# Kernel optimization log

Hardware: AMD Instinct MI355X
Metric: run time of the kernel (lower is better)

The kernel has to match this reference:

```python
import jax, jax.numpy as jnp
import numpy as np

B, T, C = 2, 4096, 512
H = 8
MEMORY = 256  # window: key j visible to query i iff 0 <= i - j <= MEMORY


def setup_inputs() -> dict:
    key = jax.random.key(0)
    k1, k2, k3 = jax.random.split(key, 3)
    x = jax.random.normal(k1, (B, T, C), dtype=jnp.float32)
    w_attn = jax.random.normal(k2, (3 * C, C), dtype=jnp.float32) * 0.02
    w_proj = jax.random.normal(k3, (C, C), dtype=jnp.float32) * 0.02
    return {"x": x, "w_attn": w_attn, "w_proj": w_proj}


def reference(x, w_attn, w_proj):
    b, t, c = x.shape
    d = c // H
    # fused QKV projection (Linear without bias): x @ W^T
    qkv = jnp.einsum('btc,fc->btf', x, w_attn)  # [B,T,3C]
    q, k, v = jnp.split(qkv, 3, axis=-1)
    # [B,T,C] -> [B,H,T,d]
    q = q.reshape(b, t, H, d).transpose(0, 2, 1, 3)
    k = k.reshape(b, t, H, d).transpose(0, 2, 1, 3)
    v = v.reshape(b, t, H, d).transpose(0, 2, 1, 3)
    # sliding-window causal mask: tril(0) & ~tril(-memory-1)
    i = jnp.arange(t)[:, None]
    j = jnp.arange(t)[None, :]
    mask = (j <= i) & (i - j <= MEMORY)  # [T,T] bool
    scores = jnp.einsum('bhqd,bhkd->bhqk', q, k) * (1.0 / np.sqrt(d))
    scores = jnp.where(mask, scores, -jnp.inf)
    attn = jax.nn.softmax(scores, axis=-1)
    y = jnp.einsum('bhqk,bhkd->bhqd', attn, v)  # [B,H,T,d]
    y = y.transpose(0, 2, 1, 3).reshape(b, t, c)
    # output projection
    y = jnp.einsum('btc,fc->btf', y, w_proj)
    return y
```

## Files before the change

kernel.cpp:

```cpp
#include <hip/hip_runtime.h>
#include <hip/hip_bf16.h>
#include <stdint.h>

#define BB 2
#define TT 4096
#define CC 512
#define HH 8
#define MEM 256

typedef unsigned short u16;
typedef __bf16 bf16x8 __attribute__((ext_vector_type(8)));
typedef float floatx4 __attribute__((ext_vector_type(4)));

__device__ inline u16 f2bf(float f) {
  uint32_t u = __float_as_uint(f);
  uint32_t r = (u + 0x7fffu + ((u >> 16) & 1u)) >> 16;
  return (u16)r;
}
__device__ inline u16 f2bf_r(float f) {
  return (u16)((__float_as_uint(f) + 0x8000u) >> 16);
}

__device__ inline void gld16(const u16* g, u16* lds) {
  __builtin_amdgcn_global_load_lds(
      (const __attribute__((address_space(1))) uint32_t*)g,
      (__attribute__((address_space(3))) uint32_t*)lds, 16, 0, 0);
}

__global__ __launch_bounds__(256) void cvt_all(const float* __restrict__ x,
                                               const float* __restrict__ wa,
                                               const float* __restrict__ wp,
                                               u16* __restrict__ xb,
                                               u16* __restrict__ wab,
                                               u16* __restrict__ wpb) {
  int i = blockIdx.x * 256 + threadIdx.x;
  const float* s; u16* d; int off;
  if (i < 1048576) { s = x; d = xb; off = i; }
  else if (i < 1245184) { s = wa; d = wab; off = i - 1048576; }
  else { s = wp; d = wpb; off = i - 1245184; }
  float4 v = *reinterpret_cast<const float4*>(s + (size_t)off * 4);
  ushort4 o;
  o.x = f2bf(v.x); o.y = f2bf(v.y); o.z = f2bf(v.z); o.w = f2bf(v.w);
  *reinterpret_cast<ushort4*>(d + (size_t)off * 4) = o;
}

template <bool OUT_F32>
__global__ __launch_bounds__(256) void gemm_bt(const u16* __restrict__ A,
                                               const u16* __restrict__ Bw,
                                               void* __restrict__ Cout,
                                               int M, int N, int K) {
  __shared__ __align__(16) u16 As[128 * 32];
  __shared__ __align__(16) u16 Bs[128 * 32];
  const int tid = threadIdx.x;
  const int w = tid >> 6, lane = tid & 63, quad = lane >> 4, l16 = lane & 15;
  const int wm = w >> 1, wn = w & 1;
  const int m0 = blockIdx.x * 128, n0 = blockIdx.y * 128;

  floatx4 acc[4][4] = {};
  const int nK = K >> 5;
  for (int kb = 0; kb < nK; ++kb) {
    const int kof = kb * 32;
    {
      int c = tid;
      gld16(A + (size_t)(m0 + (c >> 2)) * K + kof + (c & 3) * 8, As + (size_t)c * 8);
      c = tid + 256;
      gld16(A + (size_t)(m0 + (c >> 2)) * K + kof + (c & 3) * 8, As + (size_t)c * 8);
      c = tid;
      gld16(Bw + (size_t)(n0 + (c >> 2)) * K + kof + (c & 3) * 8, Bs + (size_t)c * 8);
      c = tid + 256;
      gld16(Bw + (size_t)(n0 + (c >> 2)) * K + kof + (c & 3) * 8, Bs + (size_t)c * 8);
    }
    __syncthreads();
    bf16x8 af[4], bfr[4];
#pragma unroll
    for (int i = 0; i < 4; i++)
      af[i] = *reinterpret_cast<const bf16x8*>(&As[(wm * 64 + i * 16 + l16) * 32 + quad * 8]);
#pragma unroll
    for (int i = 0; i < 4; i++)
      bfr[i] = *reinterpret_cast<const bf16x8*>(&Bs[(wn * 64 + i * 16 + l16) * 32 + quad * 8]);
#pragma unroll
    for (int mi = 0; mi < 4; mi++)
#pragma unroll
      for (int ni = 0; ni < 4; ni++)
        acc[mi][ni] = __builtin_amdgcn_mfma_f32_16x16x32_bf16(af[mi], bfr[ni], acc[mi][ni], 0, 0, 0);
    __syncthreads();
  }
#pragma unroll
  for (int mi = 0; mi < 4; mi++) {
    int row = m0 + wm * 64 + mi * 16 + quad * 4;
#pragma unroll
    for (int ni = 0; ni < 4; ni++) {
      int col = n0 + wn * 64 + ni * 16 + l16;
#pragma unroll
      for (int r = 0; r < 4; r++) {
        if (OUT_F32)
          ((float*)Cout)[(size_t)(row + r) * N + col] = acc[mi][ni][r];
        else
          ((u16*)Cout)[(size_t)(row + r) * N + col] = f2bf(acc[mi][ni][r]);
      }
    }
  }
}

__global__ __launch_bounds__(256) void gemm_bt_n64(const u16* __restrict__ A,
                                                   const u16* __restrict__ Bw,
                                                   float* __restrict__ C,
                                                   int M, int N, int K) {
  __shared__ __align__(16) u16 As[128 * 32];
  __shared__ __align__(16) u16 Bs[64 * 32];
  const int tid = threadIdx.x;
  const int w = tid >> 6, lane = tid & 63, quad = lane >> 4, l16 = lane & 15;
  const int m0 = blockIdx.x * 128, n0 = blockIdx.y * 64;

  floatx4 acc[2][4] = {};
  const int nK = K >> 5;
  for (int kb = 0; kb < nK; ++kb) {
    const int kof = kb * 32;
    {
      int c = tid;
      gld16(A + (size_t)(m0 + (c >> 2)) * K + kof + (c & 3) * 8, As + (size_t)c * 8);
      c = tid + 256;
      gld16(A + (size_t)(m0 + (c >> 2)) * K + kof + (c & 3) * 8, As + (size_t)c * 8);
      c = tid;
      gld16(Bw + (size_t)(n0 + (c >> 2)) * K + kof + (c & 3) * 8, Bs + (size_t)c * 8);
    }
    __syncthreads();
    bf16x8 af[2], bfr[4];
#pragma unroll
    for (int i = 0; i < 2; i++)
      af[i] = *reinterpret_cast<const bf16x8*>(&As[(w * 32 + i * 16 + l16) * 32 + quad * 8]);
#pragma unroll
    for (int i = 0; i < 4; i++)
      bfr[i] = *reinterpret_cast<const bf16x8*>(&Bs[(i * 16 + l16) * 32 + quad * 8]);
#pragma unroll
    for (int mi = 0; mi < 2; mi++)
#pragma unroll
      for (int ni = 0; ni < 4; ni++)
        acc[mi][ni] = __builtin_amdgcn_mfma_f32_16x16x32_bf16(af[mi], bfr[ni], acc[mi][ni], 0, 0, 0);
    __syncthreads();
  }
#pragma unroll
  for (int mi = 0; mi < 2; mi++) {
    int row = m0 + w * 32 + mi * 16 + quad * 4;
#pragma unroll
    for (int ni = 0; ni < 4; ni++) {
      int col = n0 + ni * 16 + l16;
#pragma unroll
      for (int r = 0; r < 4; r++)
        C[(size_t)(row + r) * N + col] = acc[mi][ni][r];
    }
  }
}

__global__ __launch_bounds__(256, 2) void attn_win(const u16* __restrict__ qkv,
                                                   u16* __restrict__ y) {
  const int q0 = blockIdx.x * 128;
  const int h = blockIdx.y;
  const int b = blockIdx.z;
  const int tid = threadIdx.x;
  const int w = tid >> 6, lane = tid & 63, quad = lane >> 4, l16 = lane & 15;

  __shared__ __align__(16) u16 Qs[128 * 64];
  __shared__ __align__(16) u16 Ks[64 * 64];
  __shared__ __align__(16) u16 Vt[64 * 72];
  __shared__ __align__(16) u16 Ps[4][32 * 72];

  const size_t baseQ = ((size_t)(b * TT + q0)) * 1536 + h * 64;
#pragma unroll
  for (int j = 0; j < 4; j++) {
    int c = tid + j * 256, row = c >> 3, blk = (c & 7) ^ (row & 7);
    gld16(qkv + baseQ + (size_t)row * 1536 + blk * 8, Qs + (size_t)c * 8);
  }
  __syncthreads();
  bf16x8 qf[2][2];
#pragma unroll
  for (int mi = 0; mi < 2; mi++) {
    int row = w * 32 + mi * 16 + l16;
    qf[mi][0] = *reinterpret_cast<const bf16x8*>(&Qs[row * 64 + (quad ^ (l16 & 7)) * 8]);
    qf[mi][1] = *reinterpret_cast<const bf16x8*>(&Qs[row * 64 + ((quad + 4) ^ (l16 & 7)) * 8]);
#pragma unroll
    for (int e = 0; e < 8; e++) {
      qf[mi][0][e] = qf[mi][0][e] * (__bf16)0.125f;
      qf[mi][1][e] = qf[mi][1][e] * (__bf16)0.125f;
    }
  }

  floatx4 acc_o[2][4] = {};
  float l_acc[2][4] = {{0.f, 0.f, 0.f, 0.f}, {0.f, 0.f, 0.f, 0.f}};

  const int s_min = (q0 >= 256) ? 0 : ((256 - q0) >> 6);
  const int key_v = tid >> 3, dc_v = tid & 7;
  const int key_v1 = (tid + 256) >> 3, dc_v1 = tid & 7;

  uint4 vp0, vp1;
  {
    size_t baseV = ((size_t)(b * TT + (q0 - 256 + s_min * 64))) * 1536 + 1024 + h * 64;
    vp0 = *reinterpret_cast<const uint4*>(qkv + baseV + (size_t)key_v * 1536 + dc_v * 8);
    vp1 = *reinterpret_cast<const uint4*>(qkv + baseV + (size_t)key_v1 * 1536 + dc_v1 * 8);
  }

  for (int s = s_min; s < 6; ++s) {
    const int k0 = q0 - 256 + s * 64;
    const size_t baseK = ((size_t)(b * TT + k0)) * 1536 + 512 + h * 64;
    {
      int c = tid, row = c >> 3, blk = (c & 7) ^ (row & 7);
      gld16(qkv + baseK + (size_t)row * 1536 + blk * 8, Ks + (size_t)c * 8);
      c = tid + 256; row = c >> 3; blk = (c & 7) ^ (row & 7);
      gld16(qkv + baseK + (size_t)row * 1536 + blk * 8, Ks + (size_t)c * 8);
    }
    {
      u16 tmp[8];
      *reinterpret_cast<uint4*>(tmp) = vp0;
      int col = key_v ^ (dc_v * 8);
#pragma unroll
      for (int e = 0; e < 8; e++) Vt[(dc_v * 8 + e) * 72 + col] = tmp[e];
      *reinterpret_cast<uint4*>(tmp) = vp1;
      col = key_v1 ^ (dc_v1 * 8);
#pragma unroll
      for (int e = 0; e < 8; e++) Vt[(dc_v1 * 8 + e) * 72 + col] = tmp[e];
    }
    if (s < 5) {
      size_t baseV = ((size_t)(b * TT + k0 + 64)) * 1536 + 1024 + h * 64;
      vp0 = *reinterpret_cast<const uint4*>(qkv + baseV + (size_t)key_v * 1536 + dc_v * 8);
      vp1 = *reinterpret_cast<const uint4*>(qkv + baseV + (size_t)key_v1 * 1536 + dc_v1 * 8);
    }
    __syncthreads();

    int mode = 0;
    if (s == 0) mode = (w < 2) ? 1 : 3;
    else if (s == 1) mode = (w < 2) ? 0 : 1;
    else if (s == 4) mode = (w < 2) ? 2 : 0;
    else if (s == 5) mode = (w < 2) ? 3 : 2;

    if (mode != 3) {
      bf16x8 bfr[4][2];
#pragma unroll
      for (int nt = 0; nt < 4; nt++) {
        int krow = nt * 16 + l16;
        bfr[nt][0] = *reinterpret_cast<const bf16x8*>(&Ks[krow * 64 + (quad ^ (l16 & 7)) * 8]);
        bfr[nt][1] = *reinterpret_cast<const bf16x8*>(&Ks[krow * 64 + ((quad + 4) ^ (l16 & 7)) * 8]);
      }
      floatx4 sc[2][4] = {};
#pragma unroll
      for (int mi = 0; mi < 2; mi++)
#pragma unroll
        for (int nt = 0; nt < 4; nt++) {
          sc[mi][nt] = __builtin_amdgcn_mfma_f32_16x16x32_bf16(qf[mi][0], bfr[nt][0], sc[mi][nt], 0, 0, 0);
          sc[mi][nt] = __builtin_amdgcn_mfma_f32_16x16x32_bf16(qf[mi][1], bfr[nt][1], sc[mi][nt], 0, 0, 0);
        }
      const int hqb = (w & 1) * 32 + quad * 4;
      if (mode == 1) {
#pragma unroll
        for (int mi = 0; mi < 2; mi++)
#pragma unroll
          for (int nt = 0; nt < 4; nt++)
#pragma unroll
            for (int r = 0; r < 4; r++)
              if (hqb + mi * 16 + r > nt * 16 + l16) sc[mi][nt][r] = -1e30f;
      } else if (mode == 2) {
#pragma unroll
        for (int mi = 0; mi < 2; mi++)
#pragma unroll
          for (int nt = 0; nt < 4; nt++)
#pragma unroll
            for (int r = 0; r < 4; r++)
              if (hqb + mi * 16 + r < nt * 16 + l16) sc[mi][nt][r] = -1e30f;
      }
#pragma unroll
      for (int mi = 0; mi < 2; mi++)
#pragma unroll
        for (int nt = 0; nt < 4; nt++)
#pragma unroll
          for (int r = 0; r < 4; r++) {
            float p = __expf(sc[mi][nt][r] - 4.0f);
            l_acc[mi][r] += p;
            Ps[w][(mi * 16 + quad * 4 + r) * 72 + nt * 16 + l16] = f2bf_r(p);
          }
#pragma unroll
      for (int mi = 0; mi < 2; mi++)
#pragma unroll
        for (int ki = 0; ki < 2; ki++) {
          bf16x8 pf = *reinterpret_cast<const bf16x8*>(
              &Ps[w][(mi * 16 + l16) * 72 + ki * 32 + quad * 8]);
#pragma unroll
          for (int nt = 0; nt < 4; nt++) {
            int d = nt * 16 + l16;
            bf16x8 vf = *reinterpret_cast<const bf16x8*>(
                &Vt[d * 72 + ((ki * 32 + quad * 8) ^ (d & 56))]);
            acc_o[mi][nt] = __builtin_amdgcn_mfma_f32_16x16x32_bf16(pf, vf, acc_o[mi][nt], 0, 0, 0);
          }
        }
    }
    __syncthreads();
  }
#pragma unroll
  for (int mi = 0; mi < 2; mi++)
#pragma unroll
    for (int r = 0; r < 4; r++) {
      float l = l_acc[mi][r];
      l += __shfl_xor(l, 1);
      l += __shfl_xor(l, 2);
      l += __shfl_xor(l, 4);
      l += __shfl_xor(l, 8);
      float inv = 1.f / l;
      int row = q0 + w * 32 + mi * 16 + quad * 4 + r;
      size_t base = (size_t)(b * TT + row) * 512 + h * 64;
#pragma unroll
      for (int nt = 0; nt < 4; nt++)
        y[base + nt * 16 + l16] = f2bf(acc_o[mi][nt][r] * inv);
    }
}

extern "C" void kernel_launch(void* const* d_in, const int* in_sizes, int n_in,
                              void* d_out, int out_size, void* d_ws, size_t ws_size,
                              hipStream_t stream) {
  const float* x = (const float*)d_in[0];
  const float* w_attn = (const float*)d_in[1];
  const float* w_proj = (const float*)d_in[2];
  float* out = (float*)d_out;

  u16* xb = (u16*)d_ws;
  u16* wab = xb + (size_t)8192 * 512;
  u16* wpb = wab + (size_t)1536 * 512;
  u16* qkv = wpb + (size_t)512 * 512;
  u16* yb = qkv + (size_t)8192 * 1536;

  cvt_all<<<5120, 256, 0, stream>>>(x, w_attn, w_proj, xb, wab, wpb);
  gemm_bt<false><<<dim3(64, 12), 256, 0, stream>>>(xb, wab, (void*)qkv, 8192, 1536, 512);
  attn_win<<<dim3(TT / 128, HH, BB), 256, 0, stream>>>(qkv, yb);
  gemm_bt_n64<<<dim3(64, 8), 256, 0, stream>>>(yb, wpb, out, 8192, 512, 512);
}
```

Measured before the change: 126.0 us.

## Replace QKV GEMM with 256x256 double-buffered, swizzled, phase-pipelined MFMA kernel

The 128x128 single-buffered QKV GEMM is replaced by a 512-thread kernel computing 256x256 tiles with BK=64. It double-buffers LDS, staging half-tiles across four compute phases so global loads overlap MFMA work. It also XOR-swizzles LDS to avoid bank conflicts, raises wave priority around the MFMA block, and remaps block IDs across XCDs. The tradeoffs are only 192 workgroups on a large-CU GPU, heavy LDS (128KB per block), and many more accumulator registers.

```diff
diff --git a/kernel.cpp b/kernel.cpp
--- a/kernel.cpp
+++ b/kernel.cpp
@@ -26,6 +26,8 @@
       (const __attribute__((address_space(1))) uint32_t*)g,
       (__attribute__((address_space(3))) uint32_t*)lds, 16, 0, 0);
 }
+
+#define BARM() asm volatile("" ::: "memory")
 
 __global__ __launch_bounds__(256) void cvt_all(const float* __restrict__ x,
                                                const float* __restrict__ wa,
@@ -44,60 +46,124 @@
   *reinterpret_cast<ushort4*>(d + (size_t)off * 4) = o;
 }
 
-template <bool OUT_F32>
-__global__ __launch_bounds__(256) void gemm_bt(const u16* __restrict__ A,
-                                               const u16* __restrict__ Bw,
-                                               void* __restrict__ Cout,
-                                               int M, int N, int K) {
-  __shared__ __align__(16) u16 As[128 * 32];
-  __shared__ __align__(16) u16 Bs[128 * 32];
+__device__ inline void stage_hA(const u16* __restrict__ G, u16* lds, int K,
+                                int gr0, int koff, int half, int wv, int lane) {
+#pragma unroll
+  for (int j = 0; j < 2; j++) {
+    int lrow = (j * 8 + wv) * 8 + (lane >> 3);
+    int row = (lrow & 63) + ((lrow >> 6) << 7) + (half << 6);
+    int blk = (lane & 7) ^ (row & 7);
+    gld16(G + (size_t)(gr0 + row) * K + koff + blk * 8,
+          lds + (size_t)row * 64 + (lane & 7) * 8);
+  }
+}
+__device__ inline void stage_hB(const u16* __restrict__ G, u16* lds, int K,
+                                int gr0, int koff, int half, int wv, int lane) {
+#pragma unroll
+  for (int j = 0; j < 2; j++) {
+    int lrow = (j * 8 + wv) * 8 + (lane >> 3);
+    int row = (lrow & 31) + ((lrow >> 5) << 6) + (half << 5);
+    int blk = (lane & 7) ^ (row & 7);
+    gld16(G + (size_t)(gr0 + row) * K + koff + blk * 8,
+          lds + (size_t)row * 64 + (lane & 7) * 8);
+  }
+}
+
+#define PHASE(MQ, NQ, STAGE, WAITV)                                            \
+  {                                                                            \
+    bf16x8 af[4][2], bfv[2][2];                                                \
+    _Pragma("unroll") for (int fm = 0; fm < 4; fm++) {                         \
+      int row = wm * 128 + MQ * 64 + fm * 16 + l16;                            \
+      const u16* p = Ad + (size_t)row * 64;                                    \
+      af[fm][0] = *(const bf16x8*)(p + ((quad ^ (row & 7)) << 3));             \
+      af[fm][1] = *(const bf16x8*)(p + (((4 + quad) ^ (row & 7)) << 3));       \
+    }                                                                          \
+    _Pragma("unroll") for (int fn = 0; fn < 2; fn++) {                         \
+      int row = wn * 64 + NQ * 32 + fn * 16 + l16;                             \
+      const u16* p = Bd + (size_t)row * 64;                                    \
+      bfv[fn][0] = *(const bf16x8*)(p + ((quad ^ (row & 7)) << 3));            \
+      bfv[fn][1] = *(const bf16x8*)(p + (((4 + quad) ^ (row & 7)) << 3));      \
+    }                                                                          \
+    STAGE;                                                                     \
+    BARM();                                                                    \
+    __builtin_amdgcn_s_barrier();                                              \
+    asm volatile("s_waitcnt lgkmcnt(0)" ::: "memory");                         \
+    __builtin_amdgcn_sched_barrier(0);                                         \
+    __builtin_amdgcn_s_setprio(1);                                             \
+    _Pragma("unroll") for (int fm = 0; fm < 4; fm++)                           \
+      _Pragma("unroll") for (int fn = 0; fn < 2; fn++) {                       \
+        acc[MQ * 4 + fm][NQ * 2 + fn] =                                        \
+            __builtin_amdgcn_mfma_f32_16x16x32_bf16(                           \
+                af[fm][0], bfv[fn][0], acc[MQ * 4 + fm][NQ * 2 + fn], 0, 0, 0);\
+        acc[MQ * 4 + fm][NQ * 2 + fn] =                                        \
+            __builtin_amdgcn_mfma_f32_16x16x32_bf16(                           \
+                af[fm][1], bfv[fn][1], acc[MQ * 4 + fm][NQ * 2 + fn], 0, 0, 0);\
+      }                                                                        \
+    __builtin_amdgcn_s_setprio(0);                                             \
+    WAITV;                                                                     \
+    BARM();                                                                    \
+    __builtin_amdgcn_s_barrier();                                              \
+    BARM();                                                                    \
+  }
+
+__global__ __launch_bounds__(512, 2) void gemm256(const u16* __restrict__ A,
+                                                  const u16* __restrict__ Bw,
+                                                  u16* __restrict__ C,
+                                                  int M, int N, int K) {
+  __shared__ __align__(16) u16 As[2][256 * 64];
+  __shared__ __align__(16) u16 Bs[2][256 * 64];
   const int tid = threadIdx.x;
-  const int w = tid >> 6, lane = tid & 63, quad = lane >> 4, l16 = lane & 15;
-  const int wm = w >> 1, wn = w & 1;
-  const int m0 = blockIdx.x * 128, n0 = blockIdx.y * 128;
-
-  floatx4 acc[4][4] = {};
-  const int nK = K >> 5;
-  for (int kb = 0; kb < nK; ++kb) {
-    const int kof = kb * 32;
-    {
-      int c = tid;
-      gld16(A + (size_t)(m0 + (c >> 2)) * K + kof + (c & 3) * 8, As + (size_t)c * 8);
-      c = tid + 256;
-      gld16(A + (size_t)(m0 + (c >> 2)) * K + kof + (c & 3) * 8, As + (size_t)c * 8);
-      c = tid;
-      gld16(Bw + (size_t)(n0 + (c >> 2)) * K + kof + (c & 3) * 8, Bs + (size_t)c * 8);
-      c = tid + 256;
-      gld16(Bw + (size_t)(n0 + (c >> 2)) * K + kof + (c & 3) * 8, Bs + (size_t)c * 8);
-    }
-    __syncthreads();
-    bf16x8 af[4], bfr[4];
-#pragma unroll
-    for (int i = 0; i < 4; i++)
-      af[i] = *reinterpret_cast<const bf16x8*>(&As[(wm * 64 + i * 16 + l16) * 32 + quad * 8]);
-#pragma unroll
-    for (int i = 0; i < 4; i++)
-      bfr[i] = *reinterpret_cast<const bf16x8*>(&Bs[(wn * 64 + i * 16 + l16) * 32 + quad * 8]);
-#pragma unroll
-    for (int mi = 0; mi < 4; mi++)
-#pragma unroll
-      for (int ni = 0; ni < 4; ni++)
-        acc[mi][ni] = __builtin_amdgcn_mfma_f32_16x16x32_bf16(af[mi], bfr[ni], acc[mi][ni], 0, 0, 0);
-    __syncthreads();
-  }
-#pragma unroll
-  for (int mi = 0; mi < 4; mi++) {
-    int row = m0 + wm * 64 + mi * 16 + quad * 4;
+  const int lane = tid & 63, wv = tid >> 6;
+  const int quad = lane >> 4, l16 = lane & 15;
+  const int wm = wv >> 2, wn = wv & 3;
+
+  const int nbx = N >> 8;
+  const int nwg = (M >> 8) * nbx;
+  int wg = blockIdx.x;
+  if ((nwg & 7) == 0) wg = (wg & 7) * (nwg >> 3) + (wg >> 3);
+  const int m0 = (wg / nbx) << 8, n0 = (wg % nbx) << 8;
+
+  const int nK = K >> 6;
+  floatx4 acc[8][4] = {};
+
+  stage_hA(A, As[0], K, m0, 0, 0, wv, lane);
+  stage_hA(A, As[0], K, m0, 0, 1, wv, lane);
+  stage_hB(Bw, Bs[0], K, n0, 0, 0, wv, lane);
+  stage_hB(Bw, Bs[0], K, n0, 0, 1, wv, lane);
+  if (nK > 1) {
+    stage_hA(A, As[1], K, m0, 64, 0, wv, lane);
+    stage_hB(Bw, Bs[1], K, n0, 64, 0, wv, lane);
+    asm volatile("s_waitcnt vmcnt(4)" ::: "memory");
+  } else {
+    asm volatile("s_waitcnt vmcnt(0)" ::: "memory");
+  }
+  BARM();
+  __builtin_amdgcn_s_barrier();
+  BARM();
+
+  for (int t = 0; t < nK; ++t) {
+    const int d = t & 1;
+    u16* Ad = As[d]; u16* Bd = Bs[d];
+    u16* An = As[d ^ 1]; u16* Bn = Bs[d ^ 1];
+    const int k1 = (t + 1) << 6, k2 = (t + 2) << 6;
+
+    PHASE(0, 0, { if (t + 1 < nK) stage_hA(A, An, K, m0, k1, 1, wv, lane); }, {})
+    PHASE(0, 1, { if (t + 1 < nK) stage_hB(Bw, Bn, K, n0, k1, 1, wv, lane); }, {})
+    PHASE(1, 0, { if (t + 2 < nK) stage_hA(A, Ad, K, m0, k2, 0, wv, lane); }, {})
+    PHASE(1, 1, { if (t + 2 < nK) stage_hB(Bw, Bd, K, n0, k2, 0, wv, lane); },
+          { if (t + 2 < nK) asm volatile("s_waitcnt vmcnt(4)" ::: "memory");
+            else            asm volatile("s_waitcnt vmcnt(0)" ::: "memory"); })
+  }
+
+#pragma unroll
+  for (int mi = 0; mi < 8; mi++) {
+    int row = m0 + wm * 128 + mi * 16 + quad * 4;
 #pragma unroll
     for (int ni = 0; ni < 4; ni++) {
       int col = n0 + wn * 64 + ni * 16 + l16;
 #pragma unroll
-      for (int r = 0; r < 4; r++) {
-        if (OUT_F32)
-          ((float*)Cout)[(size_t)(row + r) * N + col] = acc[mi][ni][r];
-        else
-          ((u16*)Cout)[(size_t)(row + r) * N + col] = f2bf(acc[mi][ni][r]);
-      }
+      for (int r = 0; r < 4; r++)
+        C[(size_t)(row + r) * N + col] = f2bf(acc[mi][ni][r]);
     }
   }
 }
@@ -326,7 +392,7 @@
   u16* yb = qkv + (size_t)8192 * 1536;
 
   cvt_all<<<5120, 256, 0, stream>>>(x, w_attn, w_proj, xb, wab, wpb);
-  gemm_bt<false><<<dim3(64, 12), 256, 0, stream>>>(xb, wab, (void*)qkv, 8192, 1536, 512);
+  gemm256<<<192, 512, 0, stream>>>(xb, wab, qkv, 8192, 1536, 512);
   attn_win<<<dim3(TT / 128, HH, BB), 256, 0, stream>>>(qkv, yb);
   gemm_bt_n64<<<dim3(64, 8), 256, 0, stream>>>(yb, wpb, out, 8192, 512, 512);
 }
```

Result: no change. 128.4 us (+1.9%).

## Fuse fp32-to-bf16 conversion into QKV and projection GEMM operand loads

Applied to the files above, without the earlier changes.

Removes the separate conversion kernel. The QKV GEMM now reads fp32 x and w_attn directly, converts them to bf16 in registers and writes them to swizzled LDS, and it prefetches the next K-tile into registers while the current tile's MFMAs run. The projection GEMM converts fp32 w_proj on the fly in the same way. This saves one launch and the bf16 round trip through global memory, but the GEMMs now load twice as many bytes per operand and give up the direct global-to-LDS loads for those operands.

```diff
diff --git a/kernel.cpp b/kernel.cpp
--- a/kernel.cpp
+++ b/kernel.cpp
@@ -27,64 +27,80 @@
       (__attribute__((address_space(3))) uint32_t*)lds, 16, 0, 0);
 }
 
-__global__ __launch_bounds__(256) void cvt_all(const float* __restrict__ x,
-                                               const float* __restrict__ wa,
-                                               const float* __restrict__ wp,
-                                               u16* __restrict__ xb,
-                                               u16* __restrict__ wab,
-                                               u16* __restrict__ wpb) {
-  int i = blockIdx.x * 256 + threadIdx.x;
-  const float* s; u16* d; int off;
-  if (i < 1048576) { s = x; d = xb; off = i; }
-  else if (i < 1245184) { s = wa; d = wab; off = i - 1048576; }
-  else { s = wp; d = wpb; off = i - 1245184; }
-  float4 v = *reinterpret_cast<const float4*>(s + (size_t)off * 4);
-  ushort4 o;
-  o.x = f2bf(v.x); o.y = f2bf(v.y); o.z = f2bf(v.z); o.w = f2bf(v.w);
-  *reinterpret_cast<ushort4*>(d + (size_t)off * 4) = o;
-}
-
-template <bool OUT_F32>
-__global__ __launch_bounds__(256) void gemm_bt(const u16* __restrict__ A,
-                                               const u16* __restrict__ Bw,
-                                               void* __restrict__ Cout,
-                                               int M, int N, int K) {
+#define PK8(dst, a, b)                                                   \
+  {                                                                      \
+    bf16x8 pk;                                                           \
+    pk[0] = (__bf16)(a).x; pk[1] = (__bf16)(a).y;                        \
+    pk[2] = (__bf16)(a).z; pk[3] = (__bf16)(a).w;                        \
+    pk[4] = (__bf16)(b).x; pk[5] = (__bf16)(b).y;                        \
+    pk[6] = (__bf16)(b).z; pk[7] = (__bf16)(b).w;                        \
+    *reinterpret_cast<bf16x8*>(dst) = pk;                                \
+  }
+
+__global__ __launch_bounds__(256) void gemmA(const float* __restrict__ X,
+                                             const float* __restrict__ W,
+                                             u16* __restrict__ C) {
   __shared__ __align__(16) u16 As[128 * 32];
   __shared__ __align__(16) u16 Bs[128 * 32];
   const int tid = threadIdx.x;
-  const int w = tid >> 6, lane = tid & 63, quad = lane >> 4, l16 = lane & 15;
+  const int lane = tid & 63, w = tid >> 6, quad = lane >> 4, l16 = lane & 15;
   const int wm = w >> 1, wn = w & 1;
   const int m0 = blockIdx.x * 128, n0 = blockIdx.y * 128;
 
+  const int sr = tid >> 1, sh = tid & 1;
+  const int swz = (sr ^ (sr >> 2)) & 3;
+  const float* ga = X + (size_t)(m0 + sr) * 512 + sh * 16;
+  const float* gb = W + (size_t)(n0 + sr) * 512 + sh * 16;
+  u16* wa0 = As + sr * 32 + (((sh * 2 + 0) ^ swz) << 3);
+  u16* wa1 = As + sr * 32 + (((sh * 2 + 1) ^ swz) << 3);
+  u16* wb0 = Bs + sr * 32 + (((sh * 2 + 0) ^ swz) << 3);
+  u16* wb1 = Bs + sr * 32 + (((sh * 2 + 1) ^ swz) << 3);
+  const int rsw = (quad ^ ((l16 ^ (l16 >> 2)) & 3)) << 3;
+
   floatx4 acc[4][4] = {};
-  const int nK = K >> 5;
-  for (int kb = 0; kb < nK; ++kb) {
-    const int kof = kb * 32;
-    {
-      int c = tid;
-      gld16(A + (size_t)(m0 + (c >> 2)) * K + kof + (c & 3) * 8, As + (size_t)c * 8);
-      c = tid + 256;
-      gld16(A + (size_t)(m0 + (c >> 2)) * K + kof + (c & 3) * 8, As + (size_t)c * 8);
-      c = tid;
-      gld16(Bw + (size_t)(n0 + (c >> 2)) * K + kof + (c & 3) * 8, Bs + (size_t)c * 8);
-      c = tid + 256;
-      gld16(Bw + (size_t)(n0 + (c >> 2)) * K + kof + (c & 3) * 8, Bs + (size_t)c * 8);
-    }
-    __syncthreads();
-    bf16x8 af[4], bfr[4];
+  float4 na[4], nb[4];
+#pragma unroll
+  for (int j = 0; j < 4; j++) {
+    na[j] = *(const float4*)(ga + j * 4);
+    nb[j] = *(const float4*)(gb + j * 4);
+  }
+  PK8(wa0, na[0], na[1]); PK8(wa1, na[2], na[3]);
+  PK8(wb0, nb[0], nb[1]); PK8(wb1, nb[2], nb[3]);
+  __syncthreads();
+
+  for (int t = 0; t < 16; ++t) {
+    if (t + 1 < 16) {
+      const float* pa = ga + (t + 1) * 32;
+      const float* pb = gb + (t + 1) * 32;
+#pragma unroll
+      for (int j = 0; j < 4; j++) {
+        na[j] = *(const float4*)(pa + j * 4);
+        nb[j] = *(const float4*)(pb + j * 4);
+      }
+    }
+    bf16x8 af[4], bfv[4];
 #pragma unroll
     for (int i = 0; i < 4; i++)
-      af[i] = *reinterpret_cast<const bf16x8*>(&As[(wm * 64 + i * 16 + l16) * 32 + quad * 8]);
+      af[i] = *reinterpret_cast<const bf16x8*>(
+          &As[(wm * 64 + i * 16 + l16) * 32 + rsw]);
 #pragma unroll
     for (int i = 0; i < 4; i++)
-      bfr[i] = *reinterpret_cast<const bf16x8*>(&Bs[(wn * 64 + i * 16 + l16) * 32 + quad * 8]);
+      bfv[i] = *reinterpret_cast<const bf16x8*>(
+          &Bs[(wn * 64 + i * 16 + l16) * 32 + rsw]);
 #pragma unroll
     for (int mi = 0; mi < 4; mi++)
 #pragma unroll
       for (int ni = 0; ni < 4; ni++)
-        acc[mi][ni] = __builtin_amdgcn_mfma_f32_16x16x32_bf16(af[mi], bfr[ni], acc[mi][ni], 0, 0, 0);
-    __syncthreads();
-  }
+        acc[mi][ni] = __builtin_amdgcn_mfma_f32_16x16x32_bf16(
+            af[mi], bfv[ni], acc[mi][ni], 0, 0, 0);
+    if (t + 1 < 16) {
+      __syncthreads();
+      PK8(wa0, na[0], na[1]); PK8(wa1, na[2], na[3]);
+      PK8(wb0, nb[0], nb[1]); PK8(wb1, nb[2], nb[3]);
+      __syncthreads();
+    }
+  }
+
 #pragma unroll
   for (int mi = 0; mi < 4; mi++) {
     int row = m0 + wm * 64 + mi * 16 + quad * 4;
@@ -92,62 +108,8 @@
     for (int ni = 0; ni < 4; ni++) {
       int col = n0 + wn * 64 + ni * 16 + l16;
 #pragma unroll
-      for (int r = 0; r < 4; r++) {
-        if (OUT_F32)
-          ((float*)Cout)[(size_t)(row + r) * N + col] = acc[mi][ni][r];
-        else
-          ((u16*)Cout)[(size_t)(row + r) * N + col] = f2bf(acc[mi][ni][r]);
-      }
-    }
-  }
-}
-
-__global__ __launch_bounds__(256) void gemm_bt_n64(const u16* __restrict__ A,
-                                                   const u16* __restrict__ Bw,
-                                                   float* __restrict__ C,
-                                                   int M, int N, int K) {
-  __shared__ __align__(16) u16 As[128 * 32];
-  __shared__ __align__(16) u16 Bs[64 * 32];
-  const int tid = threadIdx.x;
-  const int w = tid >> 6, lane = tid & 63, quad = lane >> 4, l16 = lane & 15;
-  const int m0 = blockIdx.x * 128, n0 = blockIdx.y * 64;
-
-  floatx4 acc[2][4] = {};
-  const int nK = K >> 5;
-  for (int kb = 0; kb < nK; ++kb) {
-    const int kof = kb * 32;
-    {
-      int c = tid;
-      gld16(A + (size_t)(m0 + (c >> 2)) * K + kof + (c & 3) * 8, As + (size_t)c * 8);
-      c = tid + 256;
-      gld16(A + (size_t)(m0 + (c >> 2)) * K + kof + (c & 3) * 8, As + (size_t)c * 8);
-      c = tid;
-      gld16(Bw + (size_t)(n0 + (c >> 2)) * K + kof + (c & 3) * 8, Bs + (size_t)c * 8);
-    }
-    __syncthreads();
-    bf16x8 af[2], bfr[4];
-#pragma unroll
-    for (int i = 0; i < 2; i++)
-      af[i] = *reinterpret_cast<const bf16x8*>(&As[(w * 32 + i * 16 + l16) * 32 + quad * 8]);
-#pragma unroll
-    for (int i = 0; i < 4; i++)
-      bfr[i] = *reinterpret_cast<const bf16x8*>(&Bs[(i * 16 + l16) * 32 + quad * 8]);
-#pragma unroll
-    for (int mi = 0; mi < 2; mi++)
-#pragma unroll
-      for (int ni = 0; ni < 4; ni++)
-        acc[mi][ni] = __builtin_amdgcn_mfma_f32_16x16x32_bf16(af[mi], bfr[ni], acc[mi][ni], 0, 0, 0);
-    __syncthreads();
-  }
-#pragma unroll
-  for (int mi = 0; mi < 2; mi++) {
-    int row = m0 + w * 32 + mi * 16 + quad * 4;
-#pragma unroll
-    for (int ni = 0; ni < 4; ni++) {
-      int col = n0 + ni * 16 + l16;
-#pragma unroll
       for (int r = 0; r < 4; r++)
-        C[(size_t)(row + r) * N + col] = acc[mi][ni][r];
+        C[(size_t)(row + r) * 1536 + col] = f2bf(acc[mi][ni][r]);
     }
   }
 }
@@ -311,6 +273,57 @@
     }
 }
 
+__global__ __launch_bounds__(256) void projW(const u16* __restrict__ A,
+                                             const float* __restrict__ W,
+                                             float* __restrict__ C) {
+  __shared__ __align__(16) u16 As[128 * 32];
+  __shared__ __align__(16) u16 Bs[64 * 32];
+  const int tid = threadIdx.x;
+  const int w = tid >> 6, lane = tid & 63, quad = lane >> 4, l16 = lane & 15;
+  const int m0 = blockIdx.x * 128, n0 = blockIdx.y * 64;
+  const int rb = tid >> 2, qk = tid & 3;
+  const float* gw = W + (size_t)(n0 + rb) * 512 + qk * 8;
+
+  floatx4 acc[2][4] = {};
+  for (int kb = 0; kb < 16; ++kb) {
+    const int kof = kb * 32;
+    float4 f0 = *(const float4*)(gw + kof);
+    float4 f1 = *(const float4*)(gw + kof + 4);
+    {
+      int c = tid;
+      gld16(A + (size_t)(m0 + (c >> 2)) * 512 + kof + (c & 3) * 8, As + (size_t)c * 8);
+      c = tid + 256;
+      gld16(A + (size_t)(m0 + (c >> 2)) * 512 + kof + (c & 3) * 8, As + (size_t)c * 8);
+    }
+    PK8(&Bs[rb * 32 + qk * 8], f0, f1);
+    __syncthreads();
+    bf16x8 af[2], bfr[4];
+#pragma unroll
+    for (int i = 0; i < 2; i++)
+      af[i] = *reinterpret_cast<const bf16x8*>(&As[(w * 32 + i * 16 + l16) * 32 + quad * 8]);
+#pragma unroll
+    for (int i = 0; i < 4; i++)
+      bfr[i] = *reinterpret_cast<const bf16x8*>(&Bs[(i * 16 + l16) * 32 + quad * 8]);
+#pragma unroll
+    for (int mi = 0; mi < 2; mi++)
+#pragma unroll
+      for (int ni = 0; ni < 4; ni++)
+        acc[mi][ni] = __builtin_amdgcn_mfma_f32_16x16x32_bf16(af[mi], bfr[ni], acc[mi][ni], 0, 0, 0);
+    __syncthreads();
+  }
+#pragma unroll
+  for (int mi = 0; mi < 2; mi++) {
+    int row = m0 + w * 32 + mi * 16 + quad * 4;
+#pragma unroll
+    for (int ni = 0; ni < 4; ni++) {
+      int col = n0 + ni * 16 + l16;
+#pragma unroll
+      for (int r = 0; r < 4; r++)
+        C[(size_t)(row + r) * 512 + col] = acc[mi][ni][r];
+    }
+  }
+}
+
 extern "C" void kernel_launch(void* const* d_in, const int* in_sizes, int n_in,
                               void* d_out, int out_size, void* d_ws, size_t ws_size,
                               hipStream_t stream) {
@@ -319,14 +332,10 @@
   const float* w_proj = (const float*)d_in[2];
   float* out = (float*)d_out;
 
-  u16* xb = (u16*)d_ws;
-  u16* wab = xb + (size_t)8192 * 512;
-  u16* wpb = wab + (size_t)1536 * 512;
-  u16* qkv = wpb + (size_t)512 * 512;
+  u16* qkv = (u16*)d_ws;
   u16* yb = qkv + (size_t)8192 * 1536;
 
-  cvt_all<<<5120, 256, 0, stream>>>(x, w_attn, w_proj, xb, wab, wpb);
-  gemm_bt<false><<<dim3(64, 12), 256, 0, stream>>>(xb, wab, (void*)qkv, 8192, 1536, 512);
+  gemmA<<<dim3(64, 12), 256, 0, stream>>>(x, w_attn, qkv);
   attn_win<<<dim3(TT / 128, HH, BB), 256, 0, stream>>>(qkv, yb);
-  gemm_bt_n64<<<dim3(64, 8), 256, 0, stream>>>(yb, wpb, out, 8192, 512, 512);
-}
+  projW<<<dim3(64, 8), 256, 0, stream>>>(yb, w_proj, out);
+}
```

New measurement: 132.9 us. 1.05x slower.
